# Kernel optimization log

Hardware: AMD Instinct MI355X
Metric: run time of the kernel (lower is better)

Reference implementation:

```python
import jax, jax.numpy as jnp
import numpy as np

D_MODEL = 1024
N_HEADS = 16
D_HEAD = D_MODEL // N_HEADS
NEG_INF = -1000000000.0


def setup_inputs() -> dict:
    key = jax.random.key(0)
    ks = jax.random.split(key, 12)
    B, S1, S2 = 2, 2048, 2048
    query = jax.random.normal(ks[0], (B, S1, D_MODEL), dtype=jnp.float32)
    k_in = jax.random.normal(ks[1], (B, S2, D_MODEL), dtype=jnp.float32)
    v_in = jax.random.normal(ks[2], (B, S2, D_MODEL), dtype=jnp.float32)
    # causal mask: True = position is masked out (filled with -1e9)
    mask = jnp.broadcast_to(jnp.triu(jnp.ones((S1, S2), dtype=bool), k=1), (B, S1, S2))
    s = 1.0 / np.sqrt(D_MODEL)
    W_q = jax.random.uniform(ks[3], (D_MODEL, D_MODEL), jnp.float32, -s, s)
    b_q = jax.random.uniform(ks[4], (D_MODEL,), jnp.float32, -s, s)
    W_k = jax.random.uniform(ks[5], (D_MODEL, D_MODEL), jnp.float32, -s, s)
    b_k = jax.random.uniform(ks[6], (D_MODEL,), jnp.float32, -s, s)
    W_v = jax.random.uniform(ks[7], (D_MODEL, D_MODEL), jnp.float32, -s, s)
    b_v = jax.random.uniform(ks[8], (D_MODEL,), jnp.float32, -s, s)
    W_o = jax.random.uniform(ks[9], (D_MODEL, D_MODEL), jnp.float32, -s, s)
    b_o = jax.random.uniform(ks[10], (D_MODEL,), jnp.float32, -s, s)
    return {"query": query, "key": k_in, "value": v_in, "mask": mask,
            "W_q": W_q, "b_q": b_q, "W_k": W_k, "b_k": b_k,
            "W_v": W_v, "b_v": b_v, "W_o": W_o, "b_o": b_o}


def reference(query, key, value, mask, W_q, b_q, W_k, b_k, W_v, b_v, W_o, b_o):
    B, S1, _ = query.shape
    S2 = key.shape[1]
    scalar = 1.0 / np.sqrt(D_HEAD)
    # projections (torch Linear: x @ W.T + b)
    Q = (query @ W_q.T + b_q).reshape(B, S1, N_HEADS, D_HEAD).transpose(0, 2, 1, 3)
    K = (key @ W_k.T + b_k).reshape(B, S2, N_HEADS, D_HEAD).transpose(0, 2, 1, 3)
    V = (value @ W_v.T + b_v).reshape(B, S2, N_HEADS, D_HEAD).transpose(0, 2, 1, 3)
    # [B, H, S1, S2]
    scores = jnp.einsum('bhqd,bhkd->bhqk', Q, K) * scalar
    scores = jnp.where(mask[:, None, :, :], NEG_INF, scores)
    probs = jax.nn.softmax(scores, axis=-1)
    attn = jnp.einsum('bhqk,bhkd->bhqd', probs, V)
    concat = attn.transpose(0, 2, 1, 3).reshape(B, S1, D_MODEL)
    return concat @ W_o.T + b_o
```

## Files before the change

### kernel.cpp

```cpp
#include <hip/hip_runtime.h>
#include <hip/hip_bf16.h>
#include <stdint.h>

typedef __bf16 bf16;
typedef __bf16 bf16x8 __attribute__((ext_vector_type(8)));
typedef float f32x4 __attribute__((ext_vector_type(4)));
typedef float f32x16 __attribute__((ext_vector_type(16)));
typedef unsigned int u32;
typedef u32 u32x4 __attribute__((ext_vector_type(4)));

#define D_MODEL 1024
#define S_LEN 2048
#define NB 2
#define NH 16
#define DH 64

__device__ __forceinline__ void gload_lds16(const bf16* g, bf16* l) {
    auto gp = reinterpret_cast<const __attribute__((address_space(1))) unsigned int*>(
        reinterpret_cast<uintptr_t>(g));
    auto lp = reinterpret_cast<__attribute__((address_space(3))) unsigned int*>(
        reinterpret_cast<uintptr_t>(l));
    __builtin_amdgcn_global_load_lds(gp, lp, 16, 0, 0);
}

__device__ __forceinline__ u32 cvtpk(float lo, float hi) {
    u32 r; asm("v_cvt_pk_bf16_f32 %0, %1, %2" : "=v"(r) : "v"(lo), "v"(hi)); return r;
}
__device__ __forceinline__ void plswap(u32& a, u32& b) {
    asm("v_permlane32_swap_b32 %0, %1" : "+v"(a), "+v"(b));
}

__global__ __launch_bounds__(256)
void cvt_all(const float* __restrict__ q, const float* __restrict__ k,
             const float* __restrict__ v, const float* __restrict__ w0,
             const float* __restrict__ w1, const float* __restrict__ w2,
             const float* __restrict__ w3,
             bf16* __restrict__ oq, bf16* __restrict__ ok, bf16* __restrict__ ov,
             bf16* __restrict__ o0, bf16* __restrict__ o1, bf16* __restrict__ o2,
             bf16* __restrict__ o3)
{
    const int bid = blockIdx.x;
    const float* in; bf16* out; int local;
    if (bid < 6144) {
        int r = bid >> 11; local = bid & 2047;
        in  = (r == 0) ? q  : (r == 1) ? k  : v;
        out = (r == 0) ? oq : (r == 1) ? ok : ov;
    } else {
        int wb = bid - 6144;
        int r = wb >> 9; local = wb & 511;
        in  = (r == 0) ? w0 : (r == 1) ? w1 : (r == 2) ? w2 : w3;
        out = (r == 0) ? o0 : (r == 1) ? o1 : (r == 2) ? o2 : o3;
    }
    const size_t i = ((size_t)local * 256 + threadIdx.x) * 8;
    f32x4 x = *(const f32x4*)(in + i);
    f32x4 y = *(const f32x4*)(in + i + 4);
    bf16x8 o;
    #pragma unroll
    for (int j = 0; j < 4; ++j) { o[j] = (bf16)x[j]; o[4 + j] = (bf16)y[j]; }
    *(bf16x8*)(out + i) = o;
}

__global__ __launch_bounds__(256, 2)
void gemm_qkv2(const bf16* __restrict__ Aq, const bf16* __restrict__ Ak, const bf16* __restrict__ Av,
               const bf16* __restrict__ Wq, const bf16* __restrict__ Wk, const bf16* __restrict__ Wv,
               const float* __restrict__ bq, const float* __restrict__ bk, const float* __restrict__ bv,
               bf16* __restrict__ Qo, bf16* __restrict__ Ko, bf16* __restrict__ VTo, float qscale)
{
    __shared__ __align__(16) char gsm[65536];
    bf16* As = (bf16*)gsm;
    bf16* Bs = (bf16*)(gsm + 32768);

    const int K = 1024;
    const int t = threadIdx.x, lane = t & 63, wid = t >> 6;
    const int nbn = 24;
    const int cpx = gridDim.x >> 3;
    const int bid = blockIdx.x;
    const int swz = (bid & 7) * cpx + (bid >> 3);
    const int bm0 = (swz / nbn) << 7;
    const int bn0 = (swz % nbn) << 7;
    const int sel = bn0 >> 10;
    const int nl  = bn0 & 1023;
    const bf16* Ap = (sel == 0) ? Aq : (sel == 1) ? Ak : Av;
    const bf16* Bp = (sel == 0) ? Wq : (sel == 1) ? Wk : Wv;
    const float* bias = (sel == 0) ? bq : (sel == 1) ? bk : bv;

    const int r16 = lane & 15, g = lane >> 4;
    const int wr = (wid >> 1) << 6;
    const int wc = (wid & 1) << 6;

    f32x4 acc[4][4] = {};

    auto stage = [&](int buf, int k0) {
        #pragma unroll
        for (int i = 0; i < 4; ++i) {
            int ch = wid * 256 + i * 64 + lane;
            int row = ch >> 3, c8 = ch & 7;
            int sc = c8 ^ (row & 7);
            gload_lds16(Ap + (size_t)(bm0 + row) * K + k0 + sc * 8, As + buf * 8192 + ch * 8);
            gload_lds16(Bp + (size_t)(nl + row) * K + k0 + sc * 8, Bs + buf * 8192 + ch * 8);
        }
    };

    int cur = 0;
    stage(0, 0);
    for (int k0 = 0; k0 < K; k0 += 64) {
        __syncthreads();
        if (k0 + 64 < K) stage(cur ^ 1, k0 + 64);
        #pragma unroll
        for (int ks = 0; ks < 2; ++ks) {
            const int cl = ks * 4 + g;
            bf16x8 af[4], bfr[4];
            #pragma unroll
            for (int mi = 0; mi < 4; ++mi) {
                int row = wr + mi * 16 + r16;
                af[mi] = *(const bf16x8*)((const char*)As + cur * 16384 + row * 128 + ((cl ^ (row & 7)) << 4));
            }
            #pragma unroll
            for (int ni = 0; ni < 4; ++ni) {
                int row = wc + ni * 16 + r16;
                bfr[ni] = *(const bf16x8*)((const char*)Bs + cur * 16384 + row * 128 + ((cl ^ (row & 7)) << 4));
            }
            #pragma unroll
            for (int mi = 0; mi < 4; ++mi)
                #pragma unroll
                for (int ni = 0; ni < 4; ++ni)
                    acc[mi][ni] = __builtin_amdgcn_mfma_f32_16x16x32_bf16(af[mi], bfr[ni], acc[mi][ni], 0, 0, 0);
        }
        cur ^= 1;
    }

    const int rb = g * 4;
    if (sel == 2) {
        __syncthreads();
        bf16* Ts = (bf16*)gsm;
        #pragma unroll
        for (int mi = 0; mi < 4; ++mi)
            #pragma unroll
            for (int ni = 0; ni < 4; ++ni) {
                int dl = wc + ni * 16 + r16;
                float bv = bias[nl + dl];
                #pragma unroll
                for (int r = 0; r < 4; ++r) {
                    int sl = wr + mi * 16 + rb + r;
                    Ts[dl * 136 + sl] = (bf16)(acc[mi][ni][r] + bv);
                }
            }
        __syncthreads();
        const int bq2 = bm0 >> 11, s0 = bm0 & 2047;
        #pragma unroll
        for (int i2 = 0; i2 < 8; ++i2) {
            int ch = t + i2 * 256;
            int d = ch >> 4, sc = ch & 15;
            int hg = (nl + d) >> 6, dl2 = (nl + d) & 63;
            bf16x8 v = *(const bf16x8*)&Ts[d * 136 + sc * 8];
            *(bf16x8*)(VTo + ((size_t)(bq2 * 16 + hg) * 64 + dl2) * S_LEN + s0 + sc * 8) = v;
        }
    } else {
        bf16* out = sel ? Ko : Qo;
        const float cs = sel ? 1.0f : qscale;
        #pragma unroll
        for (int mi = 0; mi < 4; ++mi) {
            #pragma unroll
            for (int ni = 0; ni < 4; ++ni) {
                int cg = nl + wc + ni * 16 + r16;
                float bv = bias[cg];
                #pragma unroll
                for (int r = 0; r < 4; ++r) {
                    int rg = bm0 + wr + mi * 16 + rb + r;
                    out[(size_t)rg * 1024 + cg] = (bf16)((acc[mi][ni][r] + bv) * cs);
                }
            }
        }
    }
}

__global__ __launch_bounds__(256)
void gemm_out(const bf16* __restrict__ Ap, const bf16* __restrict__ Bp,
              const float* __restrict__ bias, float* __restrict__ Cp)
{
    __shared__ __align__(16) bf16 As[2][128 * 64];
    __shared__ __align__(16) bf16 Bs[2][64 * 64];

    const int K = 1024, N = 1024;
    const int t = threadIdx.x, lane = t & 63, wid = t >> 6;
    const int nbn = 16;
    const int cpx = gridDim.x >> 3;
    const int bid = blockIdx.x;
    const int swz = (bid & 7) * cpx + (bid >> 3);
    const int bm0 = (swz / nbn) << 7;
    const int bn0 = (swz % nbn) << 6;
    const int r16 = lane & 15, g = lane >> 4;
    const int wr = (wid >> 1) << 6;
    const int wc = (wid & 1) << 5;

    f32x4 acc[4][2] = {};

    auto stage = [&](int buf, int k0) {
        #pragma unroll
        for (int i = 0; i < 4; ++i) {
            int ch = wid * 256 + i * 64 + lane;
            int row = ch >> 3, c8 = ch & 7;
            int sc = c8 ^ (row & 7);
            gload_lds16(Ap + (size_t)(bm0 + row) * K + k0 + sc * 8, &As[buf][ch * 8]);
        }
        #pragma unroll
        for (int i = 0; i < 2; ++i) {
            int ch = wid * 128 + i * 64 + lane;
            int row = ch >> 3, c8 = ch & 7;
            int sc = c8 ^ (row & 7);
            gload_lds16(Bp + (size_t)(bn0 + row) * K + k0 + sc * 8, &Bs[buf][ch * 8]);
        }
    };

    int cur = 0;
    stage(0, 0);
    for (int k0 = 0; k0 < K; k0 += 64) {
        __syncthreads();
        if (k0 + 64 < K) stage(cur ^ 1, k0 + 64);
        #pragma unroll
        for (int ks = 0; ks < 2; ++ks) {
            const int cl = ks * 4 + g;
            bf16x8 af[4], bfr[2];
            #pragma unroll
            for (int mi = 0; mi < 4; ++mi) {
                int row = wr + mi * 16 + r16;
                af[mi] = *(const bf16x8*)((const char*)&As[cur][0] + row * 128 + ((cl ^ (row & 7)) << 4));
            }
            #pragma unroll
            for (int ni = 0; ni < 2; ++ni) {
                int row = wc + ni * 16 + r16;
                bfr[ni] = *(const bf16x8*)((const char*)&Bs[cur][0] + row * 128 + ((cl ^ (row & 7)) << 4));
            }
            #pragma unroll
            for (int mi = 0; mi < 4; ++mi)
                #pragma unroll
                for (int ni = 0; ni < 2; ++ni)
                    acc[mi][ni] = __builtin_amdgcn_mfma_f32_16x16x32_bf16(af[mi], bfr[ni], acc[mi][ni], 0, 0, 0);
        }
        cur ^= 1;
    }

    const int rb = g * 4;
    #pragma unroll
    for (int mi = 0; mi < 4; ++mi) {
        #pragma unroll
        for (int ni = 0; ni < 2; ++ni) {
            int cg = bn0 + wc + ni * 16 + r16;
            float bv = bias[cg];
            #pragma unroll
            for (int r = 0; r < 4; ++r) {
                int rg = bm0 + wr + mi * 16 + rb + r;
                Cp[(size_t)rg * N + cg] = acc[mi][ni][r] + bv;
            }
        }
    }
}

__global__ __launch_bounds__(256, 2)
void attn8(const bf16* __restrict__ Qp, const bf16* __restrict__ Kp,
           const bf16* __restrict__ VTp, bf16* __restrict__ Pws, float* __restrict__ MLws)
{
    __shared__ __align__(16) char smem[2][16384];

    const int t = threadIdx.x, lane = t & 63, qs = t >> 6;
    const int l31 = lane & 31, hh = lane >> 5;

    const int bid = blockIdx.x;
    const int xcd = bid & 7, s = bid >> 3;
    const int bh = xcd * 4 + (s >> 4);
    const int rem = s & 15;
    const int kh = rem >> 3, P = rem & 7;
    const int b = bh >> 4, h = bh & 15;

    const size_t base = (size_t)b * (S_LEN * D_MODEL) + h * DH;
    const size_t vtbase = (size_t)bh * (DH * S_LEN);

    auto stage = [&](int buf, int tt) {
        char* kb = smem[buf];
        char* vb = kb + 8192;
        #pragma unroll
        for (int p = 0; p < 2; ++p) {
            int ch = t + p * 256;
            int row = ch >> 3, c8 = ch & 7;
            int so = (c8 ^ (row & 7)) << 3;
            gload_lds16(Kp + base + (size_t)(tt * 64 + row) * D_MODEL + so, (bf16*)(kb + ch * 16));
            gload_lds16(VTp + vtbase + (size_t)row * S_LEN + tt * 64 + so, (bf16*)(vb + ch * 16));
        }
    };

    #pragma unroll 1
    for (int ph = 0; ph < 2; ++ph) {
        const int qt = ph ? (15 - P) : P;
        const int q0w = qt * 128 + qs * 32;
        const int nr = qt + 1;
        const int tbase = kh ? (qt + 1) : 0;
        const int teff = 2 * qt + (qs >> 1) + 1;

        bf16x8 qf[4];
        {
            const bf16* qrow = Qp + base + (size_t)(q0w + l31) * D_MODEL + hh * 8;
            #pragma unroll
            for (int db = 0; db < 4; ++db) qf[db] = *(const bf16x8*)(qrow + db * 16);
        }

        f32x16 oacc[2] = {};
        float mx = -1e30f, lsum = 0.f;

        if (ph) __syncthreads();
        int cur = 0;
        stage(0, tbase);
        #pragma unroll 1
        for (int r = 0; r < nr; ++r) {
            __syncthreads();
            if (r + 1 < nr) stage(cur ^ 1, tbase + r + 1);
            const int tt = tbase + r;
            if (tt < teff) {
                const char* kbp = smem[cur];
                const char* vbp = kbp + 8192;
                f32x16 sacc[2] = {};
                __builtin_amdgcn_s_setprio(1);
                #pragma unroll
                for (int ks = 0; ks < 2; ++ks) {
                    int row = ks * 32 + l31;
                    #pragma unroll
                    for (int db = 0; db < 4; ++db) {
                        int c = db * 2 + hh;
                        bf16x8 kf = *(const bf16x8*)(kbp + row * 128 + ((c ^ (row & 7)) << 4));
                        sacc[ks] = __builtin_amdgcn_mfma_f32_32x32x16_bf16(kf, qf[db], sacc[ks], 0, 0, 0);
                    }
                }
                __builtin_amdgcn_s_setprio(0);
                if (tt == teff - 1) {
                    const int thr = q0w + l31 - 4 * hh - tt * 64;
                    #pragma unroll
                    for (int ks = 0; ks < 2; ++ks)
                        #pragma unroll
                        for (int r2 = 0; r2 < 16; ++r2) {
                            const int cr = 32 * ks + (r2 & 3) + 8 * (r2 >> 2);
                            if (cr > thr) sacc[ks][r2] = -1e9f;
                        }
                }
                float pm = -3e38f;
                #pragma unroll
                for (int ks = 0; ks < 2; ++ks)
                    #pragma unroll
                    for (int r2 = 0; r2 < 16; ++r2) pm = fmaxf(pm, sacc[ks][r2]);
                pm = fmaxf(pm, __shfl_xor(pm, 32));
                if (__any(pm > mx)) {
                    float mnew = fmaxf(mx, pm);
                    float al = __builtin_exp2f(mx - mnew);
                    lsum *= al;
                    #pragma unroll
                    for (int dt = 0; dt < 2; ++dt)
                        #pragma unroll
                        for (int r2 = 0; r2 < 16; ++r2) oacc[dt][r2] *= al;
                    mx = mnew;
                }
                float ts = 0.f;
                #pragma unroll
                for (int ks = 0; ks < 2; ++ks)
                    #pragma unroll
                    for (int r2 = 0; r2 < 16; ++r2) {
                        float p = __builtin_exp2f(sacc[ks][r2] - mx);
                        sacc[ks][r2] = p;
                        ts += p;
                    }
                lsum += ts + __shfl_xor(ts, 32);

                #pragma unroll
                for (int kb2 = 0; kb2 < 4; ++kb2) {
                    const int ks = kb2 >> 1, rb2 = (kb2 & 1) * 8;
                    u32 w0 = cvtpk(sacc[ks][rb2 + 0], sacc[ks][rb2 + 1]);
                    u32 w2 = cvtpk(sacc[ks][rb2 + 4], sacc[ks][rb2 + 5]);
                    u32 w1 = cvtpk(sacc[ks][rb2 + 2], sacc[ks][rb2 + 3]);
                    u32 w3 = cvtpk(sacc[ks][rb2 + 6], sacc[ks][rb2 + 7]);
                    plswap(w0, w2);
                    plswap(w1, w3);
                    u32x4 pw; pw[0] = w0; pw[1] = w1; pw[2] = w2; pw[3] = w3;
                    bf16x8 pb = __builtin_bit_cast(bf16x8, pw);
                    __builtin_amdgcn_s_setprio(1);
                    #pragma unroll
                    for (int dt = 0; dt < 2; ++dt) {
                        int row = dt * 32 + l31, c = kb2 * 2 + hh;
                        bf16x8 vfr = *(const bf16x8*)(vbp + row * 128 + ((c ^ (row & 7)) << 4));
                        oacc[dt] = __builtin_amdgcn_mfma_f32_32x32x16_bf16(vfr, pb, oacc[dt], 0, 0, 0);
                    }
                    __builtin_amdgcn_s_setprio(0);
                }
            }
            cur ^= 1;
        }

        const int pid = (bh * 16 + qt) * 2 + kh;
        bf16* pb = Pws + (size_t)pid * 8192;
        const int qrow = qs * 32 + l31;
        #pragma unroll
        for (int dt = 0; dt < 2; ++dt)
            #pragma unroll
            for (int r2 = 0; r2 < 16; r2 += 2) {
                int d = dt * 32 + (r2 & 3) + 8 * (r2 >> 2) + 4 * hh;
                *(u32*)(pb + qrow * 64 + d) = cvtpk(oacc[dt][r2], oacc[dt][r2 + 1]);
            }
        if (hh == 0) {
            MLws[(size_t)pid * 256 + qrow] = mx;
            MLws[(size_t)pid * 256 + 128 + qrow] = lsum;
        }
    }
}

__global__ __launch_bounds__(256)
void attn_merge(const bf16* __restrict__ Pws, const float* __restrict__ MLws,
                bf16* __restrict__ Ob)
{
    const int mb = blockIdx.x;
    const int bh = mb >> 4, qt = mb & 15;
    const int pidA = (bh * 16 + qt) * 2;
    const int pidB = pidA + 1;
    const int b = bh >> 4, h = bh & 15;

    const int t = threadIdx.x;
    const int q = t >> 1, dh = t & 1;
    const float mA = MLws[(size_t)pidA * 256 + q], lA = MLws[(size_t)pidA * 256 + 128 + q];
    const float mB = MLws[(size_t)pidB * 256 + q], lB = MLws[(size_t)pidB * 256 + 128 + q];
    const float m = fmaxf(mA, mB);
    float a0 = __builtin_exp2f(mA - m), a1 = __builtin_exp2f(mB - m);
    const float linv = 1.0f / (lA * a0 + lB * a1);
    a0 *= linv; a1 *= linv;
    const bf16* pA = Pws + (size_t)pidA * 8192 + q * 64 + dh * 32;
    const bf16* pB = Pws + (size_t)pidB * 8192 + q * 64 + dh * 32;
    bf16* op = Ob + (size_t)(b * S_LEN + qt * 128 + q) * D_MODEL + h * DH + dh * 32;
    #pragma unroll
    for (int j = 0; j < 4; ++j) {
        bf16x8 va = *(const bf16x8*)(pA + j * 8);
        bf16x8 vb = *(const bf16x8*)(pB + j * 8);
        bf16x8 o;
        #pragma unroll
        for (int e = 0; e < 8; ++e)
            o[e] = (bf16)(a0 * (float)va[e] + a1 * (float)vb[e]);
        *(bf16x8*)(op + j * 8) = o;
    }
}

extern "C" void kernel_launch(void* const* d_in, const int* in_sizes, int n_in,
                              void* d_out, int out_size, void* d_ws, size_t ws_size,
                              hipStream_t stream)
{
    const float* query = (const float*)d_in[0];
    const float* key   = (const float*)d_in[1];
    const float* value = (const float*)d_in[2];
    const float* W_q = (const float*)d_in[4];
    const float* b_q = (const float*)d_in[5];
    const float* W_k = (const float*)d_in[6];
    const float* b_k = (const float*)d_in[7];
    const float* W_v = (const float*)d_in[8];
    const float* b_v = (const float*)d_in[9];
    const float* W_o = (const float*)d_in[10];
    const float* b_o = (const float*)d_in[11];

    char* w = (char*)d_ws;
    const size_t MB = 1 << 20;
    bf16* qbf = (bf16*)(w);
    bf16* kbf = (bf16*)(w + 8 * MB);
    bf16* vbf = (bf16*)(w + 16 * MB);
    bf16* Qb  = (bf16*)(w + 24 * MB);
    bf16* Kb  = (bf16*)(w + 32 * MB);
    bf16* VT  = (bf16*)(w + 40 * MB);
    bf16* Wqb = (bf16*)(w + 48 * MB);
    bf16* Wkb = (bf16*)(w + 50 * MB);
    bf16* Wvb = (bf16*)(w + 52 * MB);
    bf16* Wob = (bf16*)(w + 54 * MB);
    bf16*  Pws  = (bf16*)(w);
    float* MLws = (float*)(w + 16 * MB);
    bf16*  Ob   = (bf16*)(w + 17 * MB);

    dim3 blk(256);
    cvt_all<<<dim3(8192), blk, 0, stream>>>(query, key, value, W_q, W_k, W_v, W_o,
                                            qbf, kbf, vbf, Wqb, Wkb, Wvb, Wob);

    const float qscale = 0.125f * 1.4426950408889634f;
    gemm_qkv2<<<dim3(768), blk, 0, stream>>>(qbf, kbf, vbf, Wqb, Wkb, Wvb,
                                             b_q, b_k, b_v, Qb, Kb, VT, qscale);

    attn8<<<dim3(512), blk, 0, stream>>>(Qb, Kb, VT, Pws, MLws);
    attn_merge<<<dim3(512), blk, 0, stream>>>(Pws, MLws, Ob);

    gemm_out<<<dim3(512), blk, 0, stream>>>(Ob, Wob, b_o, (float*)d_out);
}
```

Before: 112.6 us.

## Pre-pack K/V into MFMA fragment layout and use single-wave attention blocks

The QKV GEMM epilogue now writes K and V in a packed layout that matches the 32x32x16 MFMA operand fragments, so the attention kernel can load them straight from global memory into registers with no LDS staging or barriers. The attention kernel is rebuilt as 4096 single-wave blocks, each covering 32 query rows and half of the causal key range, with register double-buffering of K/V tiles. The merge kernel is adjusted to the finer 32-row partials. Dropping LDS sharing means each wave fetches K/V on its own, which raises L2 traffic, and it relies on having many small blocks to hide memory latency.

Measured after the change: 120.4 us. +6.9%, slower.

```diff
diff --git a/kernel.cpp b/kernel.cpp
--- a/kernel.cpp
+++ b/kernel.cpp
@@ -64,7 +64,7 @@
 void gemm_qkv2(const bf16* __restrict__ Aq, const bf16* __restrict__ Ak, const bf16* __restrict__ Av,
                const bf16* __restrict__ Wq, const bf16* __restrict__ Wk, const bf16* __restrict__ Wv,
                const float* __restrict__ bq, const float* __restrict__ bk, const float* __restrict__ bv,
-               bf16* __restrict__ Qo, bf16* __restrict__ Ko, bf16* __restrict__ VTo, float qscale)
+               bf16* __restrict__ Qo, bf16* __restrict__ KPo, bf16* __restrict__ VPo, float qscale)
 {
     __shared__ __align__(16) char gsm[65536];
     bf16* As = (bf16*)gsm;
@@ -130,7 +130,50 @@
     }
 
     const int rb = g * 4;
-    if (sel == 2) {
+    const int b2 = bm0 >> 11, kt0 = (bm0 & 2047) >> 5;
+    if (sel == 0) {
+        #pragma unroll
+        for (int mi = 0; mi < 4; ++mi) {
+            #pragma unroll
+            for (int ni = 0; ni < 4; ++ni) {
+                int cg = nl + wc + ni * 16 + r16;
+                float bv = bias[cg];
+                #pragma unroll
+                for (int r = 0; r < 4; ++r) {
+                    int rg = bm0 + wr + mi * 16 + rb + r;
+                    Qo[(size_t)rg * 1024 + cg] = (bf16)((acc[mi][ni][r] + bv) * qscale);
+                }
+            }
+        }
+    } else if (sel == 1) {
+        __syncthreads();
+        bf16* Ts = (bf16*)gsm;
+        #pragma unroll
+        for (int mi = 0; mi < 4; ++mi)
+            #pragma unroll
+            for (int ni = 0; ni < 4; ++ni) {
+                int dl = wc + ni * 16 + r16;
+                float bv = bias[nl + dl];
+                #pragma unroll
+                for (int r = 0; r < 4; ++r) {
+                    int sl = wr + mi * 16 + rb + r;
+                    Ts[sl * 136 + dl] = (bf16)(acc[mi][ni][r] + bv);
+                }
+            }
+        __syncthreads();
+        #pragma unroll
+        for (int i2 = 0; i2 < 8; ++i2) {
+            int ch = t + i2 * 256;
+            int hloc = ch >> 10, rem = ch & 1023;
+            int kt32loc = rem >> 8, db = (rem >> 6) & 3, ln = rem & 63;
+            int srcs = kt32loc * 32 + (ln & 31);
+            int srcd = hloc * 64 + db * 16 + (ln >> 5) * 8;
+            bf16x8 v = *(const bf16x8*)&Ts[srcs * 136 + srcd];
+            int bh2 = b2 * 16 + (nl >> 6) + hloc;
+            int kt32 = kt0 + kt32loc;
+            *(bf16x8*)(KPo + (((size_t)(bh2 * 64 + kt32) * 4 + db) * 64 + ln) * 8) = v;
+        }
+    } else {
         __syncthreads();
         bf16* Ts = (bf16*)gsm;
         #pragma unroll
@@ -146,30 +189,17 @@
                 }
             }
         __syncthreads();
-        const int bq2 = bm0 >> 11, s0 = bm0 & 2047;
         #pragma unroll
         for (int i2 = 0; i2 < 8; ++i2) {
             int ch = t + i2 * 256;
-            int d = ch >> 4, sc = ch & 15;
-            int hg = (nl + d) >> 6, dl2 = (nl + d) & 63;
-            bf16x8 v = *(const bf16x8*)&Ts[d * 136 + sc * 8];
-            *(bf16x8*)(VTo + ((size_t)(bq2 * 16 + hg) * 64 + dl2) * S_LEN + s0 + sc * 8) = v;
-        }
-    } else {
-        bf16* out = sel ? Ko : Qo;
-        const float cs = sel ? 1.0f : qscale;
-        #pragma unroll
-        for (int mi = 0; mi < 4; ++mi) {
-            #pragma unroll
-            for (int ni = 0; ni < 4; ++ni) {
-                int cg = nl + wc + ni * 16 + r16;
-                float bv = bias[cg];
-                #pragma unroll
-                for (int r = 0; r < 4; ++r) {
-                    int rg = bm0 + wr + mi * 16 + rb + r;
-                    out[(size_t)rg * 1024 + cg] = (bf16)((acc[mi][ni][r] + bv) * cs);
-                }
-            }
+            int hloc = ch >> 10, rem = ch & 1023;
+            int kt32loc = rem >> 8, kb = (rem >> 7) & 1, dt = (rem >> 6) & 1, ln = rem & 63;
+            int srcd = hloc * 64 + dt * 32 + (ln & 31);
+            int srcs = kt32loc * 32 + kb * 16 + (ln >> 5) * 8;
+            bf16x8 v = *(const bf16x8*)&Ts[srcd * 136 + srcs];
+            int bh2 = b2 * 16 + (nl >> 6) + hloc;
+            int kt32 = kt0 + kt32loc;
+            *(bf16x8*)(VPo + ((((size_t)(bh2 * 64 + kt32) * 2 + kb) * 2 + dt) * 64 + ln) * 8) = v;
         }
     }
 }
@@ -256,189 +286,158 @@
     }
 }
 
-__global__ __launch_bounds__(256, 2)
-void attn8(const bf16* __restrict__ Qp, const bf16* __restrict__ Kp,
-           const bf16* __restrict__ VTp, bf16* __restrict__ Pws, float* __restrict__ MLws)
-{
-    __shared__ __align__(16) char smem[2][16384];
-
-    const int t = threadIdx.x, lane = t & 63, qs = t >> 6;
+__global__ __launch_bounds__(64, 3)
+void attn9(const bf16* __restrict__ Qp, const bf16* __restrict__ KP,
+           const bf16* __restrict__ VP, bf16* __restrict__ Pws, float* __restrict__ MLws)
+{
+    const int lane = threadIdx.x;
     const int l31 = lane & 31, hh = lane >> 5;
 
     const int bid = blockIdx.x;
     const int xcd = bid & 7, s = bid >> 3;
-    const int bh = xcd * 4 + (s >> 4);
-    const int rem = s & 15;
-    const int kh = rem >> 3, P = rem & 7;
+    const int bh = xcd * 4 + (s & 3);
+    const int rest = s >> 2;
+    const int jd = rest >> 1, kh = rest & 1;
+    const int j = 63 - jd;
     const int b = bh >> 4, h = bh & 15;
 
-    const size_t base = (size_t)b * (S_LEN * D_MODEL) + h * DH;
-    const size_t vtbase = (size_t)bh * (DH * S_LEN);
-
-    auto stage = [&](int buf, int tt) {
-        char* kb = smem[buf];
-        char* vb = kb + 8192;
-        #pragma unroll
-        for (int p = 0; p < 2; ++p) {
-            int ch = t + p * 256;
-            int row = ch >> 3, c8 = ch & 7;
-            int so = (c8 ^ (row & 7)) << 3;
-            gload_lds16(Kp + base + (size_t)(tt * 64 + row) * D_MODEL + so, (bf16*)(kb + ch * 16));
-            gload_lds16(VTp + vtbase + (size_t)row * S_LEN + tt * 64 + so, (bf16*)(vb + ch * 16));
-        }
-    };
-
-    #pragma unroll 1
-    for (int ph = 0; ph < 2; ++ph) {
-        const int qt = ph ? (15 - P) : P;
-        const int q0w = qt * 128 + qs * 32;
-        const int nr = qt + 1;
-        const int tbase = kh ? (qt + 1) : 0;
-        const int teff = 2 * qt + (qs >> 1) + 1;
-
+    const int nA = (j + 2) >> 1;
+    const int r0 = kh ? nA : 0;
+    const int r1 = kh ? (j + 1) : nA;
+
+    f32x16 oacc[2] = {};
+    float mx = -1e30f, lsum = 0.f;
+
+    if (r0 < r1) {
         bf16x8 qf[4];
         {
-            const bf16* qrow = Qp + base + (size_t)(q0w + l31) * D_MODEL + hh * 8;
+            const bf16* qrow = Qp + ((size_t)(b * S_LEN + j * 32 + l31)) * D_MODEL + h * DH + hh * 8;
             #pragma unroll
             for (int db = 0; db < 4; ++db) qf[db] = *(const bf16x8*)(qrow + db * 16);
         }
 
-        f32x16 oacc[2] = {};
-        float mx = -1e30f, lsum = 0.f;
-
-        if (ph) __syncthreads();
-        int cur = 0;
-        stage(0, tbase);
-        #pragma unroll 1
-        for (int r = 0; r < nr; ++r) {
-            __syncthreads();
-            if (r + 1 < nr) stage(cur ^ 1, tbase + r + 1);
-            const int tt = tbase + r;
-            if (tt < teff) {
-                const char* kbp = smem[cur];
-                const char* vbp = kbp + 8192;
-                f32x16 sacc[2] = {};
+        const bf16* kp0 = KP + (size_t)bh * 131072 + lane * 8;
+        const bf16* vp0 = VP + (size_t)bh * 131072 + lane * 8;
+
+        auto loadK = [&](int tt, bf16x8 (&kf)[4]) {
+            const bf16* p = kp0 + (size_t)tt * 2048;
+            #pragma unroll
+            for (int db = 0; db < 4; ++db) kf[db] = *(const bf16x8*)(p + db * 512);
+        };
+        auto loadV = [&](int tt, bf16x8 (&vf)[4]) {
+            const bf16* p = vp0 + (size_t)tt * 2048;
+            #pragma unroll
+            for (int q2 = 0; q2 < 4; ++q2) vf[q2] = *(const bf16x8*)(p + q2 * 512);
+        };
+
+        auto process = [&](const bf16x8 (&kf)[4], const bf16x8 (&vf)[4], bool diag) {
+            f32x16 sacc = {};
+            __builtin_amdgcn_s_setprio(1);
+            #pragma unroll
+            for (int db = 0; db < 4; ++db)
+                sacc = __builtin_amdgcn_mfma_f32_32x32x16_bf16(kf[db], qf[db], sacc, 0, 0, 0);
+            __builtin_amdgcn_s_setprio(0);
+            if (diag) {
+                #pragma unroll
+                for (int r2 = 0; r2 < 16; ++r2) {
+                    int cr = (r2 & 3) + 8 * (r2 >> 2) + 4 * hh;
+                    if (cr > l31) sacc[r2] = -1e9f;
+                }
+            }
+            float pm = -3e38f;
+            #pragma unroll
+            for (int r2 = 0; r2 < 16; ++r2) pm = fmaxf(pm, sacc[r2]);
+            pm = fmaxf(pm, __shfl_xor(pm, 32));
+            if (__any(pm > mx)) {
+                float mnew = fmaxf(mx, pm);
+                float al = __builtin_exp2f(mx - mnew);
+                lsum *= al;
+                #pragma unroll
+                for (int dt = 0; dt < 2; ++dt)
+                    #pragma unroll
+                    for (int r2 = 0; r2 < 16; ++r2) oacc[dt][r2] *= al;
+                mx = mnew;
+            }
+            float ts = 0.f;
+            #pragma unroll
+            for (int r2 = 0; r2 < 16; ++r2) {
+                float p = __builtin_exp2f(sacc[r2] - mx);
+                sacc[r2] = p;
+                ts += p;
+            }
+            lsum += ts + __shfl_xor(ts, 32);
+            #pragma unroll
+            for (int kb = 0; kb < 2; ++kb) {
+                u32 w0 = cvtpk(sacc[kb * 8 + 0], sacc[kb * 8 + 1]);
+                u32 w2 = cvtpk(sacc[kb * 8 + 4], sacc[kb * 8 + 5]);
+                u32 w1 = cvtpk(sacc[kb * 8 + 2], sacc[kb * 8 + 3]);
+                u32 w3 = cvtpk(sacc[kb * 8 + 6], sacc[kb * 8 + 7]);
+                plswap(w0, w2);
+                plswap(w1, w3);
+                u32x4 pw; pw[0] = w0; pw[1] = w1; pw[2] = w2; pw[3] = w3;
+                bf16x8 pb = __builtin_bit_cast(bf16x8, pw);
                 __builtin_amdgcn_s_setprio(1);
                 #pragma unroll
-                for (int ks = 0; ks < 2; ++ks) {
-                    int row = ks * 32 + l31;
-                    #pragma unroll
-                    for (int db = 0; db < 4; ++db) {
-                        int c = db * 2 + hh;
-                        bf16x8 kf = *(const bf16x8*)(kbp + row * 128 + ((c ^ (row & 7)) << 4));
-                        sacc[ks] = __builtin_amdgcn_mfma_f32_32x32x16_bf16(kf, qf[db], sacc[ks], 0, 0, 0);
-                    }
-                }
+                for (int dt = 0; dt < 2; ++dt)
+                    oacc[dt] = __builtin_amdgcn_mfma_f32_32x32x16_bf16(vf[kb * 2 + dt], pb, oacc[dt], 0, 0, 0);
                 __builtin_amdgcn_s_setprio(0);
-                if (tt == teff - 1) {
-                    const int thr = q0w + l31 - 4 * hh - tt * 64;
-                    #pragma unroll
-                    for (int ks = 0; ks < 2; ++ks)
-                        #pragma unroll
-                        for (int r2 = 0; r2 < 16; ++r2) {
-                            const int cr = 32 * ks + (r2 & 3) + 8 * (r2 >> 2);
-                            if (cr > thr) sacc[ks][r2] = -1e9f;
-                        }
-                }
-                float pm = -3e38f;
-                #pragma unroll
-                for (int ks = 0; ks < 2; ++ks)
-                    #pragma unroll
-                    for (int r2 = 0; r2 < 16; ++r2) pm = fmaxf(pm, sacc[ks][r2]);
-                pm = fmaxf(pm, __shfl_xor(pm, 32));
-                if (__any(pm > mx)) {
-                    float mnew = fmaxf(mx, pm);
-                    float al = __builtin_exp2f(mx - mnew);
-                    lsum *= al;
-                    #pragma unroll
-                    for (int dt = 0; dt < 2; ++dt)
-                        #pragma unroll
-                        for (int r2 = 0; r2 < 16; ++r2) oacc[dt][r2] *= al;
-                    mx = mnew;
-                }
-                float ts = 0.f;
-                #pragma unroll
-                for (int ks = 0; ks < 2; ++ks)
-                    #pragma unroll
-                    for (int r2 = 0; r2 < 16; ++r2) {
-                        float p = __builtin_exp2f(sacc[ks][r2] - mx);
-                        sacc[ks][r2] = p;
-                        ts += p;
-                    }
-                lsum += ts + __shfl_xor(ts, 32);
-
-                #pragma unroll
-                for (int kb2 = 0; kb2 < 4; ++kb2) {
-                    const int ks = kb2 >> 1, rb2 = (kb2 & 1) * 8;
-                    u32 w0 = cvtpk(sacc[ks][rb2 + 0], sacc[ks][rb2 + 1]);
-                    u32 w2 = cvtpk(sacc[ks][rb2 + 4], sacc[ks][rb2 + 5]);
-                    u32 w1 = cvtpk(sacc[ks][rb2 + 2], sacc[ks][rb2 + 3]);
-                    u32 w3 = cvtpk(sacc[ks][rb2 + 6], sacc[ks][rb2 + 7]);
-                    plswap(w0, w2);
-                    plswap(w1, w3);
-                    u32x4 pw; pw[0] = w0; pw[1] = w1; pw[2] = w2; pw[3] = w3;
-                    bf16x8 pb = __builtin_bit_cast(bf16x8, pw);
-                    __builtin_amdgcn_s_setprio(1);
-                    #pragma unroll
-                    for (int dt = 0; dt < 2; ++dt) {
-                        int row = dt * 32 + l31, c = kb2 * 2 + hh;
-                        bf16x8 vfr = *(const bf16x8*)(vbp + row * 128 + ((c ^ (row & 7)) << 4));
-                        oacc[dt] = __builtin_amdgcn_mfma_f32_32x32x16_bf16(vfr, pb, oacc[dt], 0, 0, 0);
-                    }
-                    __builtin_amdgcn_s_setprio(0);
-                }
-            }
-            cur ^= 1;
-        }
-
-        const int pid = (bh * 16 + qt) * 2 + kh;
-        bf16* pb = Pws + (size_t)pid * 8192;
-        const int qrow = qs * 32 + l31;
-        #pragma unroll
-        for (int dt = 0; dt < 2; ++dt)
-            #pragma unroll
-            for (int r2 = 0; r2 < 16; r2 += 2) {
-                int d = dt * 32 + (r2 & 3) + 8 * (r2 >> 2) + 4 * hh;
-                *(u32*)(pb + qrow * 64 + d) = cvtpk(oacc[dt][r2], oacc[dt][r2 + 1]);
-            }
-        if (hh == 0) {
-            MLws[(size_t)pid * 256 + qrow] = mx;
-            MLws[(size_t)pid * 256 + 128 + qrow] = lsum;
-        }
+            }
+        };
+
+        bf16x8 kfA[4], kfB[4], vfA[4], vfB[4];
+        loadK(r0, kfA); loadV(r0, vfA);
+        int r = r0;
+        for (;;) {
+            if (r + 1 < r1) { loadK(r + 1, kfB); loadV(r + 1, vfB); }
+            process(kfA, vfA, r == j);
+            if (++r >= r1) break;
+            if (r + 1 < r1) { loadK(r + 1, kfA); loadV(r + 1, vfA); }
+            process(kfB, vfB, r == j);
+            if (++r >= r1) break;
+        }
+    }
+
+    const int pid = (bh * 64 + j) * 2 + kh;
+    bf16* pb2 = Pws + (size_t)pid * 2048;
+    #pragma unroll
+    for (int dt = 0; dt < 2; ++dt)
+        #pragma unroll
+        for (int r2 = 0; r2 < 16; r2 += 2) {
+            int d = dt * 32 + (r2 & 3) + 8 * (r2 >> 2) + 4 * hh;
+            *(u32*)(pb2 + l31 * 64 + d) = cvtpk(oacc[dt][r2], oacc[dt][r2 + 1]);
+        }
+    if (hh == 0) {
+        MLws[pid * 64 + l31] = mx;
+        MLws[pid * 64 + 32 + l31] = lsum;
     }
 }
 
 __global__ __launch_bounds__(256)
-void attn_merge(const bf16* __restrict__ Pws, const float* __restrict__ MLws,
-                bf16* __restrict__ Ob)
+void attn_merge9(const bf16* __restrict__ Pws, const float* __restrict__ MLws,
+                 bf16* __restrict__ Ob)
 {
     const int mb = blockIdx.x;
-    const int bh = mb >> 4, qt = mb & 15;
-    const int pidA = (bh * 16 + qt) * 2;
-    const int pidB = pidA + 1;
+    const int bh = mb >> 6, j = mb & 63;
     const int b = bh >> 4, h = bh & 15;
+    const int pidA = (bh * 64 + j) * 2, pidB = pidA + 1;
 
     const int t = threadIdx.x;
-    const int q = t >> 1, dh = t & 1;
-    const float mA = MLws[(size_t)pidA * 256 + q], lA = MLws[(size_t)pidA * 256 + 128 + q];
-    const float mB = MLws[(size_t)pidB * 256 + q], lB = MLws[(size_t)pidB * 256 + 128 + q];
+    const int q = t >> 3, c8 = t & 7;
+    const float mA = MLws[pidA * 64 + q], lA = MLws[pidA * 64 + 32 + q];
+    const float mB = MLws[pidB * 64 + q], lB = MLws[pidB * 64 + 32 + q];
     const float m = fmaxf(mA, mB);
     float a0 = __builtin_exp2f(mA - m), a1 = __builtin_exp2f(mB - m);
     const float linv = 1.0f / (lA * a0 + lB * a1);
     a0 *= linv; a1 *= linv;
-    const bf16* pA = Pws + (size_t)pidA * 8192 + q * 64 + dh * 32;
-    const bf16* pB = Pws + (size_t)pidB * 8192 + q * 64 + dh * 32;
-    bf16* op = Ob + (size_t)(b * S_LEN + qt * 128 + q) * D_MODEL + h * DH + dh * 32;
+    const bf16* pA = Pws + (size_t)pidA * 2048 + q * 64 + c8 * 8;
+    const bf16* pB = Pws + (size_t)pidB * 2048 + q * 64 + c8 * 8;
+    bf16x8 va = *(const bf16x8*)pA;
+    bf16x8 vb = *(const bf16x8*)pB;
+    bf16x8 o;
     #pragma unroll
-    for (int j = 0; j < 4; ++j) {
-        bf16x8 va = *(const bf16x8*)(pA + j * 8);
-        bf16x8 vb = *(const bf16x8*)(pB + j * 8);
-        bf16x8 o;
-        #pragma unroll
-        for (int e = 0; e < 8; ++e)
-            o[e] = (bf16)(a0 * (float)va[e] + a1 * (float)vb[e]);
-        *(bf16x8*)(op + j * 8) = o;
-    }
+    for (int e = 0; e < 8; ++e)
+        o[e] = (bf16)(a0 * (float)va[e] + a1 * (float)vb[e]);
+    *(bf16x8*)(Ob + ((size_t)(b * S_LEN + j * 32 + q)) * D_MODEL + h * DH + c8 * 8) = o;
 }
 
 extern "C" void kernel_launch(void* const* d_in, const int* in_sizes, int n_in,
@@ -463,8 +462,8 @@
     bf16* kbf = (bf16*)(w + 8 * MB);
     bf16* vbf = (bf16*)(w + 16 * MB);
     bf16* Qb  = (bf16*)(w + 24 * MB);
-    bf16* Kb  = (bf16*)(w + 32 * MB);
-    bf16* VT  = (bf16*)(w + 40 * MB);
+    bf16* KP  = (bf16*)(w + 32 * MB);
+    bf16* VP  = (bf16*)(w + 40 * MB);
     bf16* Wqb = (bf16*)(w + 48 * MB);
     bf16* Wkb = (bf16*)(w + 50 * MB);
     bf16* Wvb = (bf16*)(w + 52 * MB);
@@ -479,10 +478,10 @@
 
     const float qscale = 0.125f * 1.4426950408889634f;
     gemm_qkv2<<<dim3(768), blk, 0, stream>>>(qbf, kbf, vbf, Wqb, Wkb, Wvb,
-                                             b_q, b_k, b_v, Qb, Kb, VT, qscale);
-
-    attn8<<<dim3(512), blk, 0, stream>>>(Qb, Kb, VT, Pws, MLws);
-    attn_merge<<<dim3(512), blk, 0, stream>>>(Pws, MLws, Ob);
+                                             b_q, b_k, b_v, Qb, KP, VP, qscale);
+
+    attn9<<<dim3(4096), dim3(64), 0, stream>>>(Qb, KP, VP, Pws, MLws);
+    attn_merge9<<<dim3(2048), blk, 0, stream>>>(Pws, MLws, Ob);
 
     gemm_out<<<dim3(512), blk, 0, stream>>>(Ob, Wob, b_o, (float*)d_out);
 }
```
